# Performance work log

Hardware: AMD Instinct MI355X
Metric: run time of the kernel (lower is better)

The kernel has to match this reference:

```python
import jax, jax.numpy as jnp
import numpy as np

B, S, D, H, T = 512, 256, 64, 256, 50
IN = 2 * D + 1  # LSTM input dim = input_size*2+1
NSUB = 8       # RK4 substeps per output interval
TIME_OFFSET = 0.0

def _xavier(k, shape):
    fan_out, fan_in = shape
    lim = float(np.sqrt(6.0 / (fan_in + fan_out)))
    return jax.random.uniform(k, shape, minval=-lim, maxval=lim, dtype=jnp.float32)

def setup_inputs() -> dict:
    key = jax.random.key(0)
    ks = jax.random.split(key, 12)
    gaps = jax.random.uniform(ks[3], (B, T), minval=0.05, maxval=0.2, dtype=jnp.float32)
    return {
        "x": jax.random.normal(ks[0], (B, S, IN), jnp.float32),
        "lengths": jax.random.randint(ks[1], (B,), S // 2, S + 1),
        "label_feature": jax.random.normal(ks[2], (B, T, D), jnp.float32),
        "label_time": jnp.cumsum(gaps, axis=1),  # sorted per-sample times
        "label_mask": (jax.random.uniform(ks[4], (B, T, D)) < 0.2).astype(jnp.float32),
        "W_ih": _xavier(ks[5], (4 * H, IN)),
        "W_hh": _xavier(ks[6], (4 * H, H)),
        "b_ih": jnp.zeros((4 * H,), jnp.float32),
        "b_hh": jnp.zeros((4 * H,), jnp.float32),
        "Wp1": _xavier(ks[7], (H, H)), "bp1": jnp.zeros((H,), jnp.float32),
        "Wp2": _xavier(ks[8], (D, H)), "bp2": jnp.zeros((D,), jnp.float32),
        "Wd1": _xavier(ks[9], (H, D)), "bd1": jnp.zeros((H,), jnp.float32),
        "Wd2": _xavier(ks[10], (D, H)), "bd2": jnp.zeros((D,), jnp.float32),
    }

def _forward(x, label_feature, label_time, label_mask,
             W_ih, W_hh, b_ih, b_hh, Wp1, bp1, Wp2, bp2, Wd1, bd1, Wd2, bd2,
             lengths):
    # --- LSTM encoder (PyTorch gate order i, f, g, o) ---
    xW = jnp.einsum('bsi,gi->bsg', x, W_ih) + b_ih  # [B,S,4H]
    h0 = jnp.zeros((x.shape[0], H), x.dtype)
    def step(carry, xt):
        h, c = carry
        g = xt + h @ W_hh.T + b_hh
        i, f, gg, o = jnp.split(g, 4, axis=-1)
        c = jax.nn.sigmoid(f) * c + jax.nn.sigmoid(i) * jnp.tanh(gg)
        h = jax.nn.sigmoid(o) * jnp.tanh(c)
        return (h, c), h
    _, hs = jax.lax.scan(step, (h0, h0), jnp.swapaxes(xW, 0, 1))
    hs = jnp.swapaxes(hs, 0, 1)  # [B,S,H]
    # masked mean over valid timesteps
    mask = (jnp.arange(x.shape[1])[None, :] < lengths[:, None]).astype(x.dtype)
    pooled = (hs * mask[:, :, None]).sum(axis=1) / lengths[:, None].astype(x.dtype)
    # projection MLP -> initial ODE state
    y0 = jax.nn.relu(pooled @ Wp1.T + bp1) @ Wp2.T + bp2  # [B,D]
    # --- batched Neural-ODE integration (fixed-step RK4) ---
    def deriv(y):
        return jax.nn.relu(y @ Wd1.T + bd1) @ Wd2.T + bd2
    ts = label_time - TIME_OFFSET
    dts = (ts[:, 1:] - ts[:, :-1]) / NSUB  # [B,T-1]
    def interval(y, dt_b):
        dt = dt_b[:, None]
        for _ in range(NSUB):
            k1 = deriv(y)
            k2 = deriv(y + 0.5 * dt * k1)
            k3 = deriv(y + 0.5 * dt * k2)
            k4 = deriv(y + dt * k3)
            y = y + (dt / 6.0) * (k1 + 2.0 * k2 + 2.0 * k3 + k4)
        return y, y
    _, traj = jax.lax.scan(interval, y0, jnp.swapaxes(dts, 0, 1))  # [T-1,B,D]
    predict = jnp.swapaxes(jnp.concatenate([y0[None], traj], axis=0), 0, 1)  # [B,T,D]
    loss = (predict - label_feature) ** 2 * (1.0 - label_mask)
    return predict, loss

def reference(x, lengths, label_feature, label_time, label_mask,
              W_ih, W_hh, b_ih, b_hh, Wp1, bp1, Wp2, bp2, Wd1, bd1, Wd2, bd2):
    return _forward(x, label_feature, label_time, label_mask,
                    W_ih, W_hh, b_ih, b_hh, Wp1, bp1, Wp2, bp2, Wd1, bd1, Wd2, bd2,
                    lengths)
```

## Files before the change

### kernel.cpp

```cpp
#include <hip/hip_runtime.h>
#include <hip/hip_bf16.h>

#define BB 512
#define SS 256
#define HH 256
#define DD 64
#define TT 50
#define GG 1024
#define INW 129

typedef _Float16 h4 __attribute__((ext_vector_type(4)));
typedef _Float16 h8 __attribute__((ext_vector_type(8)));
typedef __fp16 hf2 __attribute__((ext_vector_type(2)));
typedef float f32x4 __attribute__((ext_vector_type(4)));
typedef unsigned int u32;

__device__ inline float sigf(float x) { return 1.f / (1.f + __expf(-x)); }
__device__ inline float tanhf_(float x) { return 1.f - 2.f / (__expf(2.f * x) + 1.f); }

__device__ inline u32 pkrtz(float a, float b) {
    hf2 h = __builtin_amdgcn_cvt_pkrtz(a, b);
    return __builtin_bit_cast(u32, h);
}

__global__ __launch_bounds__(256) void prep_kernel(
    const float* __restrict__ W_hh, const float* __restrict__ W_ih,
    const float* __restrict__ Wd1, const float* __restrict__ Wd2,
    h4* __restrict__ BhhV4, h4* __restrict__ BhhL4, h4* __restrict__ BhhS4,
    _Float16* __restrict__ Bih, h4* __restrict__ A1f4, h4* __restrict__ A2f4)
{
    int idx = blockIdx.x * 256 + threadIdx.x;
    if (idx < 65536) {
        int eh = idx & 1;
        int l = (idx >> 1) & 63;
        int ks = (idx >> 7) & 7;
        int s = (idx >> 10) & 7;
        int w = (idx >> 13) & 7;
        int g = s & 3, jt = s >> 2;
        int n = g * 256 + w * 32 + jt * 16 + (l & 15);
        int k = 32 * ks + 8 * (l >> 4) + 4 * eh;
        float4 v = *(const float4*)(W_hh + (size_t)n * HH + k);
        h4 o; o[0] = (_Float16)v.x; o[1] = (_Float16)v.y; o[2] = (_Float16)v.z; o[3] = (_Float16)v.w;
        if (ks < 4)      BhhV4[(((w * 8 + s) * 4 + ks) * 64 + l) * 2 + eh] = o;
        else if (ks < 6) BhhL4[(((w * 8 + s) * 2 + (ks - 4)) * 64 + l) * 2 + eh] = o;
        else             BhhS4[(((w * 8 + s) * 2 + (ks - 6)) * 64 + l) * 2 + eh] = o;
    } else if (idx < 106496) {
        int fj = idx - 65536;
        int eh = fj & 1;
        int l = (fj >> 1) & 63;
        int si = fj >> 7;
        int ks = si % 5;
        int ntile = si / 5;
        int n = ntile * 16 + (l & 15);
        int k = 32 * ks + 8 * (l >> 4) + 4 * eh;
        h4 o;
#pragma unroll
        for (int i = 0; i < 4; i++) {
            int kk = k + i;
            o[i] = (_Float16)((kk < INW) ? W_ih[(size_t)n * INW + kk] : 0.f);
        }
        *(h4*)(Bih + (size_t)fj * 4) = o;
    } else if (idx < 110592) {
        int fj = idx - 106496;
        int eh = fj & 1;
        int l = (fj >> 1) & 63;
        int slot = fj >> 7;
        int ks = slot & 1, t = slot >> 1;
        int row = 16 * t + (l & 15);
        int k = 32 * ks + 8 * (l >> 4) + 4 * eh;
        h4 o;
#pragma unroll
        for (int i = 0; i < 4; i++) o[i] = (_Float16)Wd1[(size_t)row * DD + k + i];
        A1f4[fj] = o;
    } else if (idx < 114688) {
        int fj = idx - 110592;
        int eh = fj & 1;
        int l = (fj >> 1) & 63;
        int slot = fj >> 7;
        int ks = slot & 7, t2 = slot >> 3;
        int row = 16 * t2 + (l & 15);
        int k = 32 * ks + 8 * (l >> 4) + 4 * eh;
        h4 o;
#pragma unroll
        for (int i = 0; i < 4; i++) o[i] = (_Float16)Wd2[(size_t)row * HH + k + i];
        A2f4[fj] = o;
    }
}

__global__ __launch_bounds__(256) void xw_kernel(
    const float* __restrict__ x, const _Float16* __restrict__ Bih,
    const float* __restrict__ b_ih, const float* __restrict__ b_hh,
    h4* __restrict__ xwf)
{
    __shared__ __align__(16) _Float16 ash[4][5][64][8];
    int tid = threadIdx.x;
    int w4 = tid >> 6, l = tid & 63;
    int bx = blockIdx.x;
    int t = bx >> 3, Bb = bx & 7;

    for (int i = tid; i < 64 * 160; i += 256) {
        int rr = i / 160, kk = i % 160;
        float v = (kk < INW) ? x[((size_t)(Bb * 64 + rr) * SS + t) * INW + kk] : 0.f;
        ash[rr >> 4][kk >> 5][(((kk & 31) >> 3) << 4) + (rr & 15)][kk & 7] = (_Float16)v;
    }
    __syncthreads();

    h8 A[4][5];
#pragma unroll
    for (int ms = 0; ms < 4; ms++)
#pragma unroll
        for (int ks = 0; ks < 5; ks++)
            A[ms][ks] = *(h8*)&ash[ms][ks][l][0];

    const h8* Bih8 = (const h8*)Bih;
    for (int nt16 = 0; nt16 < 16; nt16++) {
        int ntile = w4 * 16 + nt16;
        h8 Bv[5];
#pragma unroll
        for (int ks = 0; ks < 5; ks++) Bv[ks] = Bih8[(ntile * 5 + ks) * 64 + l];
        int nb = ntile * 16 + (l & 15);
        float bias = b_ih[nb] + b_hh[nb];
        f32x4 acc[4];
#pragma unroll
        for (int ms = 0; ms < 4; ms++) acc[ms] = (f32x4){0.f, 0.f, 0.f, 0.f};
#pragma unroll
        for (int ks = 0; ks < 5; ks++)
#pragma unroll
            for (int ms = 0; ms < 4; ms++)
                acc[ms] = __builtin_amdgcn_mfma_f32_16x16x32_f16(A[ms][ks], Bv[ks], acc[ms], 0, 0, 0);
        int slot = ((ntile & 15) >> 1) * 8 + (ntile & 1) * 4 + (ntile >> 4);
#pragma unroll
        for (int ms = 0; ms < 4; ms++) {
            int bg = Bb * 4 + ms;
            h4 o;
#pragma unroll
            for (int r = 0; r < 4; r++) o[r] = (_Float16)(acc[ms][r] + bias);
            xwf[(((size_t)bg * SS + t) * 64 + slot) * 64 + l] = o;
        }
    }
}

__global__ __launch_bounds__(512, 2) void lstm_kernel(
    const h8* __restrict__ BhhV, const h8* __restrict__ BhhL, const h8* __restrict__ BhhS,
    const h4* __restrict__ xwf, const int* __restrict__ lengths, float* __restrict__ pooled)
{
    __shared__ __align__(16) _Float16 Wlds[65536];
    __shared__ __align__(16) _Float16 hbuf[2][8][64][8];
    int tid = threadIdx.x;
    int w = tid >> 6, l = tid & 63;
    int bg = blockIdx.x;

    {
        const uint4* src = (const uint4*)BhhL;
        uint4* dst = (uint4*)Wlds;
#pragma unroll
        for (int i = 0; i < 16; i++) dst[i * 512 + tid] = src[i * 512 + tid];
    }

    h8 Wv[8][4];
#pragma unroll
    for (int s = 0; s < 8; s++)
#pragma unroll
        for (int ks = 0; ks < 4; ks++)
            Wv[s][ks] = BhhV[((w * 8 + s) * 4 + ks) * 64 + l];

    int len_[4];
    float c_[2][4], pa[2][4];
#pragma unroll
    for (int r = 0; r < 4; r++) {
        int b = 4 * (l >> 4) + r;
        len_[r] = lengths[bg * 16 + b];
#pragma unroll
        for (int jt = 0; jt < 2; jt++) { c_[jt][r] = 0.f; pa[jt][r] = 0.f; }
    }

    {
        uint4* hz = (uint4*)hbuf;
        hz[tid] = make_uint4(0, 0, 0, 0);
        hz[512 + tid] = make_uint4(0, 0, 0, 0);
    }
    __syncthreads();

    int cur = 0;
    for (int t = 0; t < SS; t++) {
        const h4* xpb = xwf + (((size_t)bg * SS + t) * 64 + w * 8) * 64 + l;
        int zoff = 0;
        asm volatile("" : "+v"(zoff));
        const h8* bS = BhhS + zoff;
#pragma unroll
        for (int jt = 0; jt < 2; jt++) {
            h4 xv[4];
#pragma unroll
            for (int g = 0; g < 4; g++) xv[g] = xpb[(jt * 4 + g) * 64];
            h8 Ws[4];
#pragma unroll
            for (int g = 0; g < 4; g++) Ws[g] = bS[((w * 8 + jt * 4 + g) * 2 + 0) * 64 + l];
            f32x4 acc[4];
#pragma unroll
            for (int g = 0; g < 4; g++) acc[g] = (f32x4){0.f, 0.f, 0.f, 0.f};
#pragma unroll
            for (int ks = 0; ks < 4; ks++) {
                h8 A = *(const h8*)&hbuf[cur][ks][l][0];
#pragma unroll
                for (int g = 0; g < 4; g++)
                    acc[g] = __builtin_amdgcn_mfma_f32_16x16x32_f16(A, Wv[jt * 4 + g][ks], acc[g], 0, 0, 0);
            }
            {
                h8 A = *(const h8*)&hbuf[cur][6][l][0];
#pragma unroll
                for (int g = 0; g < 4; g++)
                    acc[g] = __builtin_amdgcn_mfma_f32_16x16x32_f16(A, Ws[g], acc[g], 0, 0, 0);
            }
#pragma unroll
            for (int g = 0; g < 4; g++) Ws[g] = bS[((w * 8 + jt * 4 + g) * 2 + 1) * 64 + l];
#pragma unroll
            for (int ks = 4; ks < 6; ks++) {
                h8 A = *(const h8*)&hbuf[cur][ks][l][0];
#pragma unroll
                for (int g = 0; g < 4; g++) {
                    h8 Bw = *(const h8*)&Wlds[(((w * 8 + jt * 4 + g) * 2 + (ks - 4)) * 64 + l) * 8];
                    acc[g] = __builtin_amdgcn_mfma_f32_16x16x32_f16(A, Bw, acc[g], 0, 0, 0);
                }
            }
            {
                h8 A = *(const h8*)&hbuf[cur][7][l][0];
#pragma unroll
                for (int g = 0; g < 4; g++)
                    acc[g] = __builtin_amdgcn_mfma_f32_16x16x32_f16(A, Ws[g], acc[g], 0, 0, 0);
            }
#pragma unroll
            for (int r = 0; r < 4; r++) {
                float gi = acc[0][r] + (float)xv[0][r];
                float gf = acc[1][r] + (float)xv[1][r];
                float gg = acc[2][r] + (float)xv[2][r];
                float go = acc[3][r] + (float)xv[3][r];
                float cc = sigf(gf) * c_[jt][r] + sigf(gi) * tanhf_(gg);
                c_[jt][r] = cc;
                float hh = sigf(go) * tanhf_(cc);
                if (t < len_[r]) pa[jt][r] += hh;
                int b = 4 * (l >> 4) + r;
                int j = w * 32 + jt * 16 + (l & 15);
                hbuf[cur ^ 1][j >> 5][(((j & 31) >> 3) << 4) + b][j & 7] = (_Float16)hh;
            }
        }
        __syncthreads();
        cur ^= 1;
    }

#pragma unroll
    for (int jt = 0; jt < 2; jt++)
#pragma unroll
        for (int r = 0; r < 4; r++) {
            int b = 4 * (l >> 4) + r;
            int j = w * 32 + jt * 16 + (l & 15);
            pooled[(size_t)(bg * 16 + b) * HH + j] = pa[jt][r] / (float)len_[r];
        }
}

__global__ __launch_bounds__(256) void head_kernel(
    const float* __restrict__ pooled, const float* __restrict__ Wp1,
    const float* __restrict__ bp1, const float* __restrict__ Wp2,
    const float* __restrict__ bp2, float* __restrict__ y0ws)
{
    __shared__ __align__(16) float psh[HH];
    __shared__ __align__(16) float rsh[HH];
    int tid = threadIdx.x, b = blockIdx.x;
    psh[tid] = pooled[(size_t)b * HH + tid];
    __syncthreads();
    float a = bp1[tid];
    const float* wr = Wp1 + (size_t)tid * HH;
#pragma unroll 8
    for (int k = 0; k < HH; k += 4) {
        float4 w = *(const float4*)(wr + k);
        a += psh[k] * w.x + psh[k + 1] * w.y + psh[k + 2] * w.z + psh[k + 3] * w.w;
    }
    rsh[tid] = fmaxf(a, 0.f);
    __syncthreads();
    if (tid < DD) {
        float acc = bp2[tid];
        const float* w2 = Wp2 + (size_t)tid * HH;
#pragma unroll 8
        for (int h = 0; h < HH; h += 4) {
            float4 w = *(const float4*)(w2 + h);
            acc += rsh[h] * w.x + rsh[h + 1] * w.y + rsh[h + 2] * w.z + rsh[h + 3] * w.w;
        }
        y0ws[(size_t)b * DD + tid] = acc;
    }
}

__global__ __launch_bounds__(256) void ode_kernel(
    const float* __restrict__ y0ws, const h8* __restrict__ A1f,
    const float* __restrict__ bd1, const h8* __restrict__ A2f,
    const float* __restrict__ bd2, const float* __restrict__ ltime,
    const float* __restrict__ lfeat, const float* __restrict__ lmask,
    float* __restrict__ pred, float* __restrict__ losso)
{
    __shared__ __align__(16) _Float16 hX[4096];
    __shared__ __align__(16) _Float16 kX[1024];
    int tid = threadIdx.x;
    int wv = tid >> 6, l = tid & 63;
    int q = l >> 4, bb = l & 15;
    int b = blockIdx.x;

    h8 A1[4][2];
#pragma unroll
    for (int tt = 0; tt < 4; tt++)
#pragma unroll
        for (int ks = 0; ks < 2; ks++)
            A1[tt][ks] = A1f[((4 * wv + tt) * 2 + ks) * 64 + l];
    h8 A2[8];
#pragma unroll
    for (int ks = 0; ks < 8; ks++) A2[ks] = A2f[(wv * 8 + ks) * 64 + l];

    float bd1c[4][4];
#pragma unroll
    for (int tt = 0; tt < 4; tt++)
#pragma unroll
        for (int r = 0; r < 4; r++) bd1c[tt][r] = bd1[16 * (4 * wv + tt) + 4 * q + r];
    float bd2c[4];
#pragma unroll
    for (int r = 0; r < 4; r++) bd2c[r] = bd2[16 * wv + 4 * q + r];

    float y[16], kp[16], ksum[16];
#pragma unroll
    for (int ks = 0; ks < 2; ks++)
#pragma unroll
        for (int e = 0; e < 8; e++) {
            y[ks * 8 + e] = y0ws[(size_t)b * DD + 32 * ks + 8 * q + e];
            kp[ks * 8 + e] = 0.f;
        }

    if (wv == 0 && bb == 0) {
#pragma unroll
        for (int ks = 0; ks < 2; ks++) {
            size_t idx = ((size_t)b * TT + 0) * DD + 32 * ks + 8 * q;
            float4 p0 = make_float4(y[ks * 8 + 0], y[ks * 8 + 1], y[ks * 8 + 2], y[ks * 8 + 3]);
            float4 p1 = make_float4(y[ks * 8 + 4], y[ks * 8 + 5], y[ks * 8 + 6], y[ks * 8 + 7]);
            *(float4*)&pred[idx] = p0;
            *(float4*)&pred[idx + 4] = p1;
            float4 lf0 = *(const float4*)&lfeat[idx], lf1 = *(const float4*)&lfeat[idx + 4];
            float4 lm0 = *(const float4*)&lmask[idx], lm1 = *(const float4*)&lmask[idx + 4];
            float4 lo0, lo1;
            lo0.x = (p0.x - lf0.x) * (p0.x - lf0.x) * (1.f - lm0.x);
            lo0.y = (p0.y - lf0.y) * (p0.y - lf0.y) * (1.f - lm0.y);
            lo0.z = (p0.z - lf0.z) * (p0.z - lf0.z) * (1.f - lm0.z);
            lo0.w = (p0.w - lf0.w) * (p0.w - lf0.w) * (1.f - lm0.w);
            lo1.x = (p1.x - lf1.x) * (p1.x - lf1.x) * (1.f - lm1.x);
            lo1.y = (p1.y - lf1.y) * (p1.y - lf1.y) * (1.f - lm1.y);
            lo1.z = (p1.z - lf1.z) * (p1.z - lf1.z) * (1.f - lm1.z);
            lo1.w = (p1.w - lf1.w) * (p1.w - lf1.w) * (1.f - lm1.w);
            *(float4*)&losso[idx] = lo0;
            *(float4*)&losso[idx + 4] = lo1;
        }
    }

    for (int iv = 0; iv < TT - 1; iv++) {
        float t0 = ltime[(size_t)b * TT + iv], t1 = ltime[(size_t)b * TT + iv + 1];
        float dt = (t1 - t0) * 0.125f;
        for (int ss = 0; ss < 8; ss++) {
#pragma unroll
            for (int i = 0; i < 16; i++) ksum[i] = 0.f;
            const float AE[4] = {0.f, 0.5f, 0.5f, 1.f};
            const float WE[4] = {1.f, 2.f, 2.f, 1.f};
#pragma unroll
            for (int e = 0; e < 4; e++) {
                h8 B1[2];
#pragma unroll
                for (int ks = 0; ks < 2; ks++) {
                    float ye[8];
#pragma unroll
                    for (int i = 0; i < 8; i++) ye[i] = y[ks * 8 + i] + AE[e] * dt * kp[ks * 8 + i];
                    uint4 u;
                    u.x = pkrtz(ye[0], ye[1]); u.y = pkrtz(ye[2], ye[3]);
                    u.z = pkrtz(ye[4], ye[5]); u.w = pkrtz(ye[6], ye[7]);
                    B1[ks] = __builtin_bit_cast(h8, u);
                }
                f32x4 C1[4];
#pragma unroll
                for (int tt = 0; tt < 4; tt++) C1[tt] = (f32x4){0.f, 0.f, 0.f, 0.f};
#pragma unroll
                for (int ks = 0; ks < 2; ks++)
#pragma unroll
                    for (int tt = 0; tt < 4; tt++)
                        C1[tt] = __builtin_amdgcn_mfma_f32_16x16x32_f16(A1[tt][ks], B1[ks], C1[tt], 0, 0, 0);
#pragma unroll
                for (int tt = 0; tt < 4; tt++) {
                    float h0 = fmaxf(C1[tt][0] + bd1c[tt][0], 0.f);
                    float h1 = fmaxf(C1[tt][1] + bd1c[tt][1], 0.f);
                    float h2 = fmaxf(C1[tt][2] + bd1c[tt][2], 0.f);
                    float h3 = fmaxf(C1[tt][3] + bd1c[tt][3], 0.f);
                    int i0 = 16 * (4 * wv + tt) + 4 * q;
                    int idx = (bb * 256 + i0) ^ ((bb & 7) << 3);
                    *(uint2*)&hX[idx] = make_uint2(pkrtz(h0, h1), pkrtz(h2, h3));
                }
                __syncthreads();
                f32x4 Ca = (f32x4){0.f, 0.f, 0.f, 0.f}, Cb = (f32x4){0.f, 0.f, 0.f, 0.f};
#pragma unroll
                for (int ks = 0; ks < 8; ks += 2) {
                    h8 B2a = *(const h8*)&hX[(bb * 256 + 32 * ks + 8 * q) ^ ((bb & 7) << 3)];
                    h8 B2b = *(const h8*)&hX[(bb * 256 + 32 * (ks + 1) + 8 * q) ^ ((bb & 7) << 3)];
                    Ca = __builtin_amdgcn_mfma_f32_16x16x32_f16(A2[ks], B2a, Ca, 0, 0, 0);
                    Cb = __builtin_amdgcn_mfma_f32_16x16x32_f16(A2[ks + 1], B2b, Cb, 0, 0, 0);
                }
                {
                    float k0 = Ca[0] + Cb[0] + bd2c[0];
                    float k1 = Ca[1] + Cb[1] + bd2c[1];
                    float k2 = Ca[2] + Cb[2] + bd2c[2];
                    float k3 = Ca[3] + Cb[3] + bd2c[3];
                    int j0 = 16 * wv + 4 * q;
                    int idx = (bb * 64 + j0) ^ ((bb & 7) << 3);
                    *(uint2*)&kX[idx] = make_uint2(pkrtz(k0, k1), pkrtz(k2, k3));
                }
                __syncthreads();
#pragma unroll
                for (int ks = 0; ks < 2; ks++) {
                    h8 kvh = *(const h8*)&kX[(bb * 64 + 32 * ks + 8 * q) ^ ((bb & 7) << 3)];
#pragma unroll
                    for (int i = 0; i < 8; i++) {
                        float kvf = (float)kvh[i];
                        kp[ks * 8 + i] = kvf;
                        ksum[ks * 8 + i] += WE[e] * kvf;
                    }
                }
            }
#pragma unroll
            for (int i = 0; i < 16; i++) y[i] += dt * (1.f / 6.f) * ksum[i];
        }
        if (wv == 0 && bb == 0) {
#pragma unroll
            for (int ks = 0; ks < 2; ks++) {
                size_t idx = ((size_t)b * TT + iv + 1) * DD + 32 * ks + 8 * q;
                float4 p0 = make_float4(y[ks * 8 + 0], y[ks * 8 + 1], y[ks * 8 + 2], y[ks * 8 + 3]);
                float4 p1 = make_float4(y[ks * 8 + 4], y[ks * 8 + 5], y[ks * 8 + 6], y[ks * 8 + 7]);
                *(float4*)&pred[idx] = p0;
                *(float4*)&pred[idx + 4] = p1;
                float4 lf0 = *(const float4*)&lfeat[idx], lf1 = *(const float4*)&lfeat[idx + 4];
                float4 lm0 = *(const float4*)&lmask[idx], lm1 = *(const float4*)&lmask[idx + 4];
                float4 lo0, lo1;
                lo0.x = (p0.x - lf0.x) * (p0.x - lf0.x) * (1.f - lm0.x);
                lo0.y = (p0.y - lf0.y) * (p0.y - lf0.y) * (1.f - lm0.y);
                lo0.z = (p0.z - lf0.z) * (p0.z - lf0.z) * (1.f - lm0.z);
                lo0.w = (p0.w - lf0.w) * (p0.w - lf0.w) * (1.f - lm0.w);
                lo1.x = (p1.x - lf1.x) * (p1.x - lf1.x) * (1.f - lm1.x);
                lo1.y = (p1.y - lf1.y) * (p1.y - lf1.y) * (1.f - lm1.y);
                lo1.z = (p1.z - lf1.z) * (p1.z - lf1.z) * (1.f - lm1.z);
                lo1.w = (p1.w - lf1.w) * (p1.w - lf1.w) * (1.f - lm1.w);
                *(float4*)&losso[idx] = lo0;
                *(float4*)&losso[idx + 4] = lo1;
            }
        }
    }
}

extern "C" void kernel_launch(void* const* d_in, const int* in_sizes, int n_in,
                              void* d_out, int out_size, void* d_ws, size_t ws_size,
                              hipStream_t stream)
{
    const float* x      = (const float*)d_in[0];
    const int* lengths  = (const int*)d_in[1];
    const float* lfeat  = (const float*)d_in[2];
    const float* ltime  = (const float*)d_in[3];
    const float* lmask  = (const float*)d_in[4];
    const float* W_ih   = (const float*)d_in[5];
    const float* W_hh   = (const float*)d_in[6];
    const float* b_ih   = (const float*)d_in[7];
    const float* b_hh   = (const float*)d_in[8];
    const float* Wp1    = (const float*)d_in[9];
    const float* bp1    = (const float*)d_in[10];
    const float* Wp2    = (const float*)d_in[11];
    const float* bp2    = (const float*)d_in[12];
    const float* Wd1    = (const float*)d_in[13];
    const float* bd1    = (const float*)d_in[14];
    const float* Wd2    = (const float*)d_in[15];
    const float* bd2    = (const float*)d_in[16];

    float* pred  = (float*)d_out;
    float* losso = pred + (size_t)BB * TT * DD;

    char* ws = (char*)d_ws;
    h4*       xwf    = (h4*)(ws + 0);
    h4*       BhhV   = (h4*)(ws + 268435456);
    h4*       BhhL   = (h4*)(ws + 268697600);
    h4*       BhhS   = (h4*)(ws + 268828672);
    _Float16* Bih    = (_Float16*)(ws + 268959744);
    float*    pooled = (float*)(ws + 269287424);
    float*    y0ws   = (float*)(ws + 269811712);
    h4*       A1f    = (h4*)(ws + 269942784);
    h4*       A2f    = (h4*)(ws + 269975552);

    prep_kernel<<<448, 256, 0, stream>>>(W_hh, W_ih, Wd1, Wd2, BhhV, BhhL, BhhS, Bih, A1f, A2f);
    xw_kernel<<<2048, 256, 0, stream>>>(x, Bih, b_ih, b_hh, xwf);
    lstm_kernel<<<32, 512, 0, stream>>>((const h8*)BhhV, (const h8*)BhhL, (const h8*)BhhS,
                                        xwf, lengths, pooled);
    head_kernel<<<BB, 256, 0, stream>>>(pooled, Wp1, bp1, Wp2, bp2, y0ws);
    ode_kernel<<<512, 256, 0, stream>>>(y0ws, (const h8*)A1f, bd1, (const h8*)A2f, bd2,
                                        ltime, lfeat, lmask, pred, losso);
}
```

Measured before the change: 2.561 ms.

## Batch 16 samples per single-wave ODE block instead of one sample per block

The ODE kernel used to launch one 256-thread block per sample and filled all 16 MFMA columns with copies of that one sample. It now launches 32 single-wavefront blocks, each carrying 16 distinct samples in the MFMA N dimension, so every wave holds all weight tiles and runs both matmul layers alone. Biases are folded into the accumulator initialisation, and the XOR-swizzled LDS layout is replaced by padded rows. This removes the 16x redundant compute and the cross-wave barriers, but leaves only 32 waves on the GPU with long serial MFMA chains, much higher register pressure, and an added barrier per RK stage.

```diff
diff --git a/kernel.cpp b/kernel.cpp
--- a/kernel.cpp
+++ b/kernel.cpp
@@ -288,69 +288,71 @@
     }
 }
 
-__global__ __launch_bounds__(256) void ode_kernel(
+__global__ __launch_bounds__(64, 1) void ode_kernel(
     const float* __restrict__ y0ws, const h8* __restrict__ A1f,
     const float* __restrict__ bd1, const h8* __restrict__ A2f,
     const float* __restrict__ bd2, const float* __restrict__ ltime,
     const float* __restrict__ lfeat, const float* __restrict__ lmask,
     float* __restrict__ pred, float* __restrict__ losso)
 {
-    __shared__ __align__(16) _Float16 hX[4096];
-    __shared__ __align__(16) _Float16 kX[1024];
-    int tid = threadIdx.x;
-    int wv = tid >> 6, l = tid & 63;
+    __shared__ __align__(16) _Float16 hX[16 * 264];
+    __shared__ __align__(16) _Float16 kX[16 * 80];
+    int l = threadIdx.x;
     int q = l >> 4, bb = l & 15;
-    int b = blockIdx.x;
-
-    h8 A1[4][2];
-#pragma unroll
-    for (int tt = 0; tt < 4; tt++)
+    int bg = blockIdx.x;
+    int b = bg * 16 + bb;
+
+    h8 A1[16][2];
+#pragma unroll
+    for (int tt = 0; tt < 16; tt++)
 #pragma unroll
         for (int ks = 0; ks < 2; ks++)
-            A1[tt][ks] = A1f[((4 * wv + tt) * 2 + ks) * 64 + l];
-    h8 A2[8];
-#pragma unroll
-    for (int ks = 0; ks < 8; ks++) A2[ks] = A2f[(wv * 8 + ks) * 64 + l];
-
-    float bd1c[4][4];
-#pragma unroll
-    for (int tt = 0; tt < 4; tt++)
-#pragma unroll
-        for (int r = 0; r < 4; r++) bd1c[tt][r] = bd1[16 * (4 * wv + tt) + 4 * q + r];
-    float bd2c[4];
-#pragma unroll
-    for (int r = 0; r < 4; r++) bd2c[r] = bd2[16 * wv + 4 * q + r];
+            A1[tt][ks] = A1f[(tt * 2 + ks) * 64 + l];
+    h8 A2[4][8];
+#pragma unroll
+    for (int t2 = 0; t2 < 4; t2++)
+#pragma unroll
+        for (int ks = 0; ks < 8; ks++)
+            A2[t2][ks] = A2f[(t2 * 8 + ks) * 64 + l];
+
+    f32x4 BD1[16], BD2[4];
+#pragma unroll
+    for (int tt = 0; tt < 16; tt++)
+#pragma unroll
+        for (int r = 0; r < 4; r++) BD1[tt][r] = bd1[16 * tt + 4 * q + r];
+#pragma unroll
+    for (int t2 = 0; t2 < 4; t2++)
+#pragma unroll
+        for (int r = 0; r < 4; r++) BD2[t2][r] = bd2[16 * t2 + 4 * q + r];
 
     float y[16], kp[16], ksum[16];
 #pragma unroll
-    for (int ks = 0; ks < 2; ks++)
-#pragma unroll
-        for (int e = 0; e < 8; e++) {
-            y[ks * 8 + e] = y0ws[(size_t)b * DD + 32 * ks + 8 * q + e];
-            kp[ks * 8 + e] = 0.f;
-        }
-
-    if (wv == 0 && bb == 0) {
-#pragma unroll
-        for (int ks = 0; ks < 2; ks++) {
-            size_t idx = ((size_t)b * TT + 0) * DD + 32 * ks + 8 * q;
-            float4 p0 = make_float4(y[ks * 8 + 0], y[ks * 8 + 1], y[ks * 8 + 2], y[ks * 8 + 3]);
-            float4 p1 = make_float4(y[ks * 8 + 4], y[ks * 8 + 5], y[ks * 8 + 6], y[ks * 8 + 7]);
-            *(float4*)&pred[idx] = p0;
-            *(float4*)&pred[idx + 4] = p1;
-            float4 lf0 = *(const float4*)&lfeat[idx], lf1 = *(const float4*)&lfeat[idx + 4];
-            float4 lm0 = *(const float4*)&lmask[idx], lm1 = *(const float4*)&lmask[idx + 4];
-            float4 lo0, lo1;
-            lo0.x = (p0.x - lf0.x) * (p0.x - lf0.x) * (1.f - lm0.x);
-            lo0.y = (p0.y - lf0.y) * (p0.y - lf0.y) * (1.f - lm0.y);
-            lo0.z = (p0.z - lf0.z) * (p0.z - lf0.z) * (1.f - lm0.z);
-            lo0.w = (p0.w - lf0.w) * (p0.w - lf0.w) * (1.f - lm0.w);
-            lo1.x = (p1.x - lf1.x) * (p1.x - lf1.x) * (1.f - lm1.x);
-            lo1.y = (p1.y - lf1.y) * (p1.y - lf1.y) * (1.f - lm1.y);
-            lo1.z = (p1.z - lf1.z) * (p1.z - lf1.z) * (1.f - lm1.z);
-            lo1.w = (p1.w - lf1.w) * (p1.w - lf1.w) * (1.f - lm1.w);
-            *(float4*)&losso[idx] = lo0;
-            *(float4*)&losso[idx + 4] = lo1;
+    for (int ks2 = 0; ks2 < 2; ks2++) {
+        float4 y0a = *(const float4*)&y0ws[(size_t)b * DD + 32 * ks2 + 8 * q];
+        float4 y0b = *(const float4*)&y0ws[(size_t)b * DD + 32 * ks2 + 8 * q + 4];
+        y[ks2 * 8 + 0] = y0a.x; y[ks2 * 8 + 1] = y0a.y; y[ks2 * 8 + 2] = y0a.z; y[ks2 * 8 + 3] = y0a.w;
+        y[ks2 * 8 + 4] = y0b.x; y[ks2 * 8 + 5] = y0b.y; y[ks2 * 8 + 6] = y0b.z; y[ks2 * 8 + 7] = y0b.w;
+#pragma unroll
+        for (int e = 0; e < 8; e++) kp[ks2 * 8 + e] = 0.f;
+    }
+
+#pragma unroll
+    for (int ks2 = 0; ks2 < 2; ks2++) {
+        size_t idx = ((size_t)b * TT + 0) * DD + 32 * ks2 + 8 * q;
+#pragma unroll
+        for (int h4i = 0; h4i < 2; h4i++) {
+            float4 p;
+            p.x = y[ks2 * 8 + 4 * h4i + 0]; p.y = y[ks2 * 8 + 4 * h4i + 1];
+            p.z = y[ks2 * 8 + 4 * h4i + 2]; p.w = y[ks2 * 8 + 4 * h4i + 3];
+            *(float4*)&pred[idx + 4 * h4i] = p;
+            float4 lf = *(const float4*)&lfeat[idx + 4 * h4i];
+            float4 lm = *(const float4*)&lmask[idx + 4 * h4i];
+            float4 lo;
+            lo.x = (p.x - lf.x) * (p.x - lf.x) * (1.f - lm.x);
+            lo.y = (p.y - lf.y) * (p.y - lf.y) * (1.f - lm.y);
+            lo.z = (p.z - lf.z) * (p.z - lf.z) * (1.f - lm.z);
+            lo.w = (p.w - lf.w) * (p.w - lf.w) * (1.f - lm.w);
+            *(float4*)&losso[idx + 4 * h4i] = lo;
         }
     }
 
@@ -364,89 +366,76 @@
             const float WE[4] = {1.f, 2.f, 2.f, 1.f};
 #pragma unroll
             for (int e = 0; e < 4; e++) {
+                float adt = AE[e] * dt;
                 h8 B1[2];
 #pragma unroll
-                for (int ks = 0; ks < 2; ks++) {
-                    float ye[8];
-#pragma unroll
-                    for (int i = 0; i < 8; i++) ye[i] = y[ks * 8 + i] + AE[e] * dt * kp[ks * 8 + i];
+                for (int ks2 = 0; ks2 < 2; ks2++) {
                     uint4 u;
-                    u.x = pkrtz(ye[0], ye[1]); u.y = pkrtz(ye[2], ye[3]);
-                    u.z = pkrtz(ye[4], ye[5]); u.w = pkrtz(ye[6], ye[7]);
-                    B1[ks] = __builtin_bit_cast(h8, u);
-                }
-                f32x4 C1[4];
-#pragma unroll
-                for (int tt = 0; tt < 4; tt++) C1[tt] = (f32x4){0.f, 0.f, 0.f, 0.f};
-#pragma unroll
-                for (int ks = 0; ks < 2; ks++)
-#pragma unroll
-                    for (int tt = 0; tt < 4; tt++)
-                        C1[tt] = __builtin_amdgcn_mfma_f32_16x16x32_f16(A1[tt][ks], B1[ks], C1[tt], 0, 0, 0);
-#pragma unroll
-                for (int tt = 0; tt < 4; tt++) {
-                    float h0 = fmaxf(C1[tt][0] + bd1c[tt][0], 0.f);
-                    float h1 = fmaxf(C1[tt][1] + bd1c[tt][1], 0.f);
-                    float h2 = fmaxf(C1[tt][2] + bd1c[tt][2], 0.f);
-                    float h3 = fmaxf(C1[tt][3] + bd1c[tt][3], 0.f);
-                    int i0 = 16 * (4 * wv + tt) + 4 * q;
-                    int idx = (bb * 256 + i0) ^ ((bb & 7) << 3);
-                    *(uint2*)&hX[idx] = make_uint2(pkrtz(h0, h1), pkrtz(h2, h3));
+                    u.x = pkrtz(y[ks2 * 8 + 0] + adt * kp[ks2 * 8 + 0], y[ks2 * 8 + 1] + adt * kp[ks2 * 8 + 1]);
+                    u.y = pkrtz(y[ks2 * 8 + 2] + adt * kp[ks2 * 8 + 2], y[ks2 * 8 + 3] + adt * kp[ks2 * 8 + 3]);
+                    u.z = pkrtz(y[ks2 * 8 + 4] + adt * kp[ks2 * 8 + 4], y[ks2 * 8 + 5] + adt * kp[ks2 * 8 + 5]);
+                    u.w = pkrtz(y[ks2 * 8 + 6] + adt * kp[ks2 * 8 + 6], y[ks2 * 8 + 7] + adt * kp[ks2 * 8 + 7]);
+                    B1[ks2] = __builtin_bit_cast(h8, u);
+                }
+#pragma unroll
+                for (int tt = 0; tt < 16; tt++) {
+                    f32x4 C = BD1[tt];
+                    C = __builtin_amdgcn_mfma_f32_16x16x32_f16(A1[tt][0], B1[0], C, 0, 0, 0);
+                    C = __builtin_amdgcn_mfma_f32_16x16x32_f16(A1[tt][1], B1[1], C, 0, 0, 0);
+                    u32 p0 = pkrtz(fmaxf(C[0], 0.f), fmaxf(C[1], 0.f));
+                    u32 p1 = pkrtz(fmaxf(C[2], 0.f), fmaxf(C[3], 0.f));
+                    *(uint2*)&hX[bb * 264 + 16 * tt + 4 * q] = make_uint2(p0, p1);
                 }
                 __syncthreads();
-                f32x4 Ca = (f32x4){0.f, 0.f, 0.f, 0.f}, Cb = (f32x4){0.f, 0.f, 0.f, 0.f};
-#pragma unroll
-                for (int ks = 0; ks < 8; ks += 2) {
-                    h8 B2a = *(const h8*)&hX[(bb * 256 + 32 * ks + 8 * q) ^ ((bb & 7) << 3)];
-                    h8 B2b = *(const h8*)&hX[(bb * 256 + 32 * (ks + 1) + 8 * q) ^ ((bb & 7) << 3)];
-                    Ca = __builtin_amdgcn_mfma_f32_16x16x32_f16(A2[ks], B2a, Ca, 0, 0, 0);
-                    Cb = __builtin_amdgcn_mfma_f32_16x16x32_f16(A2[ks + 1], B2b, Cb, 0, 0, 0);
-                }
-                {
-                    float k0 = Ca[0] + Cb[0] + bd2c[0];
-                    float k1 = Ca[1] + Cb[1] + bd2c[1];
-                    float k2 = Ca[2] + Cb[2] + bd2c[2];
-                    float k3 = Ca[3] + Cb[3] + bd2c[3];
-                    int j0 = 16 * wv + 4 * q;
-                    int idx = (bb * 64 + j0) ^ ((bb & 7) << 3);
-                    *(uint2*)&kX[idx] = make_uint2(pkrtz(k0, k1), pkrtz(k2, k3));
+                f32x4 C2[4];
+#pragma unroll
+                for (int t2 = 0; t2 < 4; t2++) C2[t2] = BD2[t2];
+#pragma unroll
+                for (int ksi = 0; ksi < 8; ksi++) {
+                    h8 B2 = *(const h8*)&hX[bb * 264 + 32 * ksi + 8 * q];
+#pragma unroll
+                    for (int t2 = 0; t2 < 4; t2++)
+                        C2[t2] = __builtin_amdgcn_mfma_f32_16x16x32_f16(A2[t2][ksi], B2, C2[t2], 0, 0, 0);
+                }
+#pragma unroll
+                for (int t2 = 0; t2 < 4; t2++) {
+                    u32 p0 = pkrtz(C2[t2][0], C2[t2][1]);
+                    u32 p1 = pkrtz(C2[t2][2], C2[t2][3]);
+                    *(uint2*)&kX[bb * 80 + 16 * t2 + 4 * q] = make_uint2(p0, p1);
                 }
                 __syncthreads();
 #pragma unroll
-                for (int ks = 0; ks < 2; ks++) {
-                    h8 kvh = *(const h8*)&kX[(bb * 64 + 32 * ks + 8 * q) ^ ((bb & 7) << 3)];
-#pragma unroll
-                    for (int i = 0; i < 8; i++) {
-                        float kvf = (float)kvh[i];
-                        kp[ks * 8 + i] = kvf;
-                        ksum[ks * 8 + i] += WE[e] * kvf;
+                for (int ks2 = 0; ks2 < 2; ks2++) {
+                    h8 kf = *(const h8*)&kX[bb * 80 + 32 * ks2 + 8 * q];
+#pragma unroll
+                    for (int e2 = 0; e2 < 8; e2++) {
+                        float kv = (float)kf[e2];
+                        kp[ks2 * 8 + e2] = kv;
+                        ksum[ks2 * 8 + e2] += WE[e] * kv;
                     }
                 }
+                __syncthreads();
             }
 #pragma unroll
             for (int i = 0; i < 16; i++) y[i] += dt * (1.f / 6.f) * ksum[i];
         }
-        if (wv == 0 && bb == 0) {
-#pragma unroll
-            for (int ks = 0; ks < 2; ks++) {
-                size_t idx = ((size_t)b * TT + iv + 1) * DD + 32 * ks + 8 * q;
-                float4 p0 = make_float4(y[ks * 8 + 0], y[ks * 8 + 1], y[ks * 8 + 2], y[ks * 8 + 3]);
-                float4 p1 = make_float4(y[ks * 8 + 4], y[ks * 8 + 5], y[ks * 8 + 6], y[ks * 8 + 7]);
-                *(float4*)&pred[idx] = p0;
-                *(float4*)&pred[idx + 4] = p1;
-                float4 lf0 = *(const float4*)&lfeat[idx], lf1 = *(const float4*)&lfeat[idx + 4];
-                float4 lm0 = *(const float4*)&lmask[idx], lm1 = *(const float4*)&lmask[idx + 4];
-                float4 lo0, lo1;
-                lo0.x = (p0.x - lf0.x) * (p0.x - lf0.x) * (1.f - lm0.x);
-                lo0.y = (p0.y - lf0.y) * (p0.y - lf0.y) * (1.f - lm0.y);
-                lo0.z = (p0.z - lf0.z) * (p0.z - lf0.z) * (1.f - lm0.z);
-                lo0.w = (p0.w - lf0.w) * (p0.w - lf0.w) * (1.f - lm0.w);
-                lo1.x = (p1.x - lf1.x) * (p1.x - lf1.x) * (1.f - lm1.x);
-                lo1.y = (p1.y - lf1.y) * (p1.y - lf1.y) * (1.f - lm1.y);
-                lo1.z = (p1.z - lf1.z) * (p1.z - lf1.z) * (1.f - lm1.z);
-                lo1.w = (p1.w - lf1.w) * (p1.w - lf1.w) * (1.f - lm1.w);
-                *(float4*)&losso[idx] = lo0;
-                *(float4*)&losso[idx + 4] = lo1;
+#pragma unroll
+        for (int ks2 = 0; ks2 < 2; ks2++) {
+            size_t idx = ((size_t)b * TT + iv + 1) * DD + 32 * ks2 + 8 * q;
+#pragma unroll
+            for (int h4i = 0; h4i < 2; h4i++) {
+                float4 p;
+                p.x = y[ks2 * 8 + 4 * h4i + 0]; p.y = y[ks2 * 8 + 4 * h4i + 1];
+                p.z = y[ks2 * 8 + 4 * h4i + 2]; p.w = y[ks2 * 8 + 4 * h4i + 3];
+                *(float4*)&pred[idx + 4 * h4i] = p;
+                float4 lf = *(const float4*)&lfeat[idx + 4 * h4i];
+                float4 lm = *(const float4*)&lmask[idx + 4 * h4i];
+                float4 lo;
+                lo.x = (p.x - lf.x) * (p.x - lf.x) * (1.f - lm.x);
+                lo.y = (p.y - lf.y) * (p.y - lf.y) * (1.f - lm.y);
+                lo.z = (p.z - lf.z) * (p.z - lf.z) * (1.f - lm.z);
+                lo.w = (p.w - lf.w) * (p.w - lf.w) * (1.f - lm.w);
+                *(float4*)&losso[idx + 4 * h4i] = lo;
             }
         }
     }
@@ -493,6 +482,6 @@
     lstm_kernel<<<32, 512, 0, stream>>>((const h8*)BhhV, (const h8*)BhhL, (const h8*)BhhS,
                                         xwf, lengths, pooled);
     head_kernel<<<BB, 256, 0, stream>>>(pooled, Wp1, bp1, Wp2, bp2, y0ws);
-    ode_kernel<<<512, 256, 0, stream>>>(y0ws, (const h8*)A1f, bd1, (const h8*)A2f, bd2,
-                                        ltime, lfeat, lmask, pred, losso);
-}
+    ode_kernel<<<32, 64, 0, stream>>>(y0ws, (const h8*)A1f, bd1, (const h8*)A2f, bd2,
+                                      ltime, lfeat, lmask, pred, losso);
+}
```

After: 3.497 ms. 36.6% more time.
